# Kernel optimization log

Measured on AMD Instinct MI355X. Metric: run time of the kernel, lower is better.

## Reference

```python
import jax, jax.numpy as jnp
import numpy as np

H, NH, NKV, HD, I = 4096, 32, 8, 128, 14336
B, S = 1, 2048
THETA = 500000.0
EPS = 1e-5
SCALE = HD ** -0.5


def setup_inputs() -> dict:
    key = jax.random.key(0)
    ks = jax.random.split(key, 8)
    sc = 0.02
    return {
        "positions": jnp.arange(S, dtype=jnp.int32),
        "hidden_states": jax.random.normal(ks[0], (B, S, H), jnp.float32),
        "residual": jax.random.normal(ks[1], (B, S, H), jnp.float32),
        "w_qkv": jax.random.normal(ks[2], ((NH + 2 * NKV) * HD, H), jnp.float32) * sc,
        "w_o": jax.random.normal(ks[3], (H, NH * HD), jnp.float32) * sc,
        "w_gate_up": jax.random.normal(ks[4], (2 * I, H), jnp.float32) * sc,
        "w_down": jax.random.normal(ks[5], (H, I), jnp.float32) * sc,
        "w_ln1": jnp.ones((H,), jnp.float32),
        "w_ln2": jnp.ones((H,), jnp.float32),
    }


def rmsnorm(x, w):
    xf = x.astype(jnp.float32)
    y = xf * jax.lax.rsqrt(jnp.mean(xf * xf, axis=-1, keepdims=True) + EPS)
    return (y * w).astype(x.dtype)


def apply_rope(x, positions):
    # x: [B, S, nh, HD]; neox style: rotate halves
    half = HD // 2
    inv_freq = 1.0 / (THETA ** (jnp.arange(0, half, dtype=jnp.float32) / half))
    freqs = positions.astype(jnp.float32)[:, None] * inv_freq[None, :]  # [S, half]
    cos = jnp.cos(freqs)[None, :, None, :]
    sin = jnp.sin(freqs)[None, :, None, :]
    x1, x2 = x[..., :half], x[..., half:]
    return jnp.concatenate([x1 * cos - x2 * sin, x2 * cos + x1 * sin], axis=-1)


def reference(positions, hidden_states, residual, w_qkv, w_o, w_gate_up, w_down, w_ln1, w_ln2):
    # fused add + RMSNorm (input_layernorm with residual)
    residual = hidden_states + residual
    h = rmsnorm(residual, w_ln1)

    # fused QKV projection
    qkv = jnp.einsum('bsh,oh->bso', h, w_qkv)
    q = qkv[..., : NH * HD].reshape(B, S, NH, HD)
    k = qkv[..., NH * HD: (NH + NKV) * HD].reshape(B, S, NKV, HD)
    v = qkv[..., (NH + NKV) * HD:].reshape(B, S, NKV, HD)

    q = apply_rope(q, positions)
    k = apply_rope(k, positions)

    # GQA: expand kv heads
    rep = NH // NKV
    k = jnp.repeat(k, rep, axis=2)  # [B,S,NH,HD]
    v = jnp.repeat(v, rep, axis=2)

    scores = jnp.einsum('bqhd,bkhd->bhqk', q, k) * SCALE
    causal = jnp.tril(jnp.ones((S, S), bool))
    scores = jnp.where(causal[None, None], scores, jnp.float32(-1e30))
    attn = jax.nn.softmax(scores, axis=-1)
    ctx = jnp.einsum('bhqk,bkhd->bqhd', attn, v).reshape(B, S, NH * HD)
    attn_out = jnp.einsum('bso,ho->bsh', ctx, w_o)

    # fused add + RMSNorm (post_attention_layernorm)
    residual = attn_out + residual
    h = rmsnorm(residual, w_ln2)

    # SwiGLU MLP
    gu = jnp.einsum('bsh,oh->bso', h, w_gate_up)
    gate, up = gu[..., :I], gu[..., I:]
    h = jax.nn.silu(gate) * up
    out = jnp.einsum('bsi,hi->bsh', h, w_down)
    return out, residual
```

## Files before the change

kernel.cpp:

```cpp
#include <hip/hip_runtime.h>

typedef short bf16x8 __attribute__((ext_vector_type(8)));
typedef short short4v __attribute__((ext_vector_type(4)));
typedef float f32x4 __attribute__((ext_vector_type(4)));

#define SCALE_ATTN 0.08838834764831845f

__device__ inline short f2bs(float f) {
    unsigned u = __builtin_bit_cast(unsigned, f);
    unsigned r = (u + 0x7fffu + ((u >> 16) & 1u)) >> 16;
    return (short)(unsigned short)r;
}
__device__ inline float b2f(short s) {
    unsigned u = ((unsigned)(unsigned short)s) << 16;
    return __builtin_bit_cast(float, u);
}
__device__ inline void pack_w4(const f32x4& a, const f32x4& b, bf16x8& p) {
    p[0] = f2bs(a[0]); p[1] = f2bs(a[1]); p[2] = f2bs(a[2]); p[3] = f2bs(a[3]);
    p[4] = f2bs(b[0]); p[5] = f2bs(b[1]); p[6] = f2bs(b[2]); p[7] = f2bs(b[3]);
}

__global__ __launch_bounds__(256)
void wconv_kernel(const float* __restrict__ src, short* __restrict__ dst, long n8)
{
    const long stride = (long)gridDim.x << 8;
    for (long i = ((long)blockIdx.x << 8) + threadIdx.x; i < n8; i += stride) {
        const f32x4 a = __builtin_nontemporal_load(&((const f32x4*)src)[i << 1]);
        const f32x4 b = __builtin_nontemporal_load(&((const f32x4*)src)[(i << 1) + 1]);
        bf16x8 p;
        pack_w4(a, b, p);
        ((bf16x8*)dst)[i] = p;
    }
}

__global__ __launch_bounds__(512)
void wconv_gu_kernel(const float* __restrict__ src, short* __restrict__ dst)
{
    const int n = blockIdx.x;
    const int t = n >> 8, r = n & 255;
    const int orig = (r < 128) ? (t * 128 + r) : (14336 + t * 128 + (r - 128));
    const float* s = src + (long)orig * 4096;
    short* d = dst + (long)n * 4096;
    const int j = threadIdx.x << 3;
    f32x4 a = __builtin_nontemporal_load((const f32x4*)(s + j));
    f32x4 b = __builtin_nontemporal_load((const f32x4*)(s + j + 4));
    bf16x8 p; pack_w4(a, b, p);
    *(bf16x8*)(d + j) = p;
}

__global__ __launch_bounds__(256)
void add_rmsnorm_kernel(const float* __restrict__ X, const float* __restrict__ X2,
                        const float* __restrict__ Rin, const float* __restrict__ w,
                        float* __restrict__ Rout, short* __restrict__ Hout)
{
    const int tid = threadIdx.x;
    const long base = (long)blockIdx.x << 12;
    float v[16];
    float ss = 0.f;
#pragma unroll
    for (int p = 0; p < 4; ++p) {
        const int idx = (p << 10) + (tid << 2);
        f32x4 a = *(const f32x4*)(X + base + idx);
        if (X2 != nullptr) {
            f32x4 b = *(const f32x4*)(X2 + base + idx);
            a += b;
        }
        if (Rin != nullptr) {
            f32x4 b = *(const f32x4*)(Rin + base + idx);
            a += b;
        }
        v[p*4+0] = a[0]; v[p*4+1] = a[1]; v[p*4+2] = a[2]; v[p*4+3] = a[3];
        ss += a[0]*a[0] + a[1]*a[1] + a[2]*a[2] + a[3]*a[3];
    }
#pragma unroll
    for (int dd = 1; dd < 64; dd <<= 1) ss += __shfl_xor(ss, dd);
    __shared__ float red[4];
    if ((tid & 63) == 0) red[tid >> 6] = ss;
    __syncthreads();
    const float tot = red[0] + red[1] + red[2] + red[3];
    const float rstd = rsqrtf(tot * (1.0f / 4096.0f) + 1e-5f);
#pragma unroll
    for (int p = 0; p < 4; ++p) {
        const int idx = (p << 10) + (tid << 2);
        if (Rout != nullptr) {
            f32x4 b;
            b[0] = v[p*4+0]; b[1] = v[p*4+1]; b[2] = v[p*4+2]; b[3] = v[p*4+3];
            *(f32x4*)(Rout + base + idx) = b;
        }
        f32x4 wv4 = *(const f32x4*)(w + idx);
        short4v hb;
        hb[0] = f2bs(v[p*4+0] * rstd * wv4[0]);
        hb[1] = f2bs(v[p*4+1] * rstd * wv4[1]);
        hb[2] = f2bs(v[p*4+2] * rstd * wv4[2]);
        hb[3] = f2bs(v[p*4+3] * rstd * wv4[3]);
        *(short4v*)(Hout + base + idx) = hb;
    }
}

__global__ __launch_bounds__(256)
void add2_kernel(const float* __restrict__ a, const float* __restrict__ b,
                 float* __restrict__ o, long n4)
{
    const long st = (long)gridDim.x << 8;
    for (long i = ((long)blockIdx.x << 8) + threadIdx.x; i < n4; i += st) {
        f32x4 x = __builtin_nontemporal_load(&((const f32x4*)a)[i]);
        f32x4 y = __builtin_nontemporal_load(&((const f32x4*)b)[i]);
        x += y;
        ((f32x4*)o)[i] = x;
    }
}

#define BAR()   do { asm volatile("" ::: "memory"); __builtin_amdgcn_s_barrier(); asm volatile("" ::: "memory"); } while (0)
#define LGKM0() asm volatile("s_waitcnt lgkmcnt(0)" ::: "memory")
#define VMW(n)  asm volatile("s_waitcnt vmcnt(" #n ")" ::: "memory")

__device__ inline bf16x8 lds_frag(const short* tile, int row, int kb) {
    const int off = row * 128 + (kb ^ ((row & 7) << 4));
    return *(const bf16x8*)((const char*)tile + off);
}

__device__ inline void stage_half(const short* __restrict__ G, long grow0, long K,
                                  long k0, short* ldsHalf, int wv, int lane)
{
#pragma unroll
    for (int i = 0; i < 2; ++i) {
        short* dst = ldsHalf + ((i << 13) + (wv << 10)) / 2;
        const int off = (wv << 10) + (i << 13) + (lane << 4);
        const int r   = off >> 7;
        const int cb  = off & 127;
        const int gcb = cb ^ ((r & 7) << 4);
        const short* src = G + (grow0 + r) * K + k0 + (gcb >> 1);
        __builtin_amdgcn_global_load_lds(
            (const __attribute__((address_space(1))) void*)(const void*)src,
            (__attribute__((address_space(3))) void*)(void*)dst, 16, 0, 0);
    }
}

#define LOAD_A(T, grp) do {                                        \
    _Pragma("unroll") for (int _m = 0; _m < 4; ++_m) {             \
        const int _row = abase + (grp)*64 + _m*16 + l15;           \
        a[_m][0] = lds_frag(T, _row, l4b);                         \
        a[_m][1] = lds_frag(T, _row, 64 + l4b);                    \
    } } while (0)

#define LOAD_B(T, n0) do {                                         \
    _Pragma("unroll") for (int _n = 0; _n < 2; ++_n) {             \
        const int _row = bbase + ((n0)+_n)*16 + l15;               \
        b[(n0)+_n][0] = lds_frag(T, _row, l4b);                    \
        b[(n0)+_n][1] = lds_frag(T, _row, 64 + l4b);               \
    } } while (0)

#define MFMA16(MB, NB) do {                                                        \
    __builtin_amdgcn_s_setprio(1);                                                 \
    _Pragma("unroll") for (int _m = 0; _m < 4; ++_m)                               \
    _Pragma("unroll") for (int _n = 0; _n < 2; ++_n) {                             \
        acc[(MB)+_m][(NB)+_n] = __builtin_amdgcn_mfma_f32_16x16x32_bf16(           \
            a[_m][0], b[(NB)+_n][0], acc[(MB)+_m][(NB)+_n], 0, 0, 0);              \
        acc[(MB)+_m][(NB)+_n] = __builtin_amdgcn_mfma_f32_16x16x32_bf16(           \
            a[_m][1], b[(NB)+_n][1], acc[(MB)+_m][(NB)+_n], 0, 0, 0);              \
    }                                                                              \
    __builtin_amdgcn_s_setprio(0);                                                 \
} while (0)

template<int EPI, int KS>
__global__ __launch_bounds__(512, 2)
void gemm8(const short* __restrict__ A, const short* __restrict__ W,
           float* __restrict__ Cf, short* __restrict__ Cb,
           int N, int K)
{
    __shared__ __align__(16) short As[2][16384];
    __shared__ __align__(16) short Bs[2][16384];

    const int tid  = threadIdx.x;
    const int lane = tid & 63;
    const int wv   = tid >> 6;
    const int wm   = wv >> 2;
    const int wn   = wv & 3;
    const int l15  = lane & 15;
    const int l4b  = (lane >> 4) << 4;

    const int gx   = gridDim.x;
    const int nwg  = gx * 8 * KS;
    const int cpx  = nwg >> 3;
    const int orig = (blockIdx.z * 8 + blockIdx.y) * gx + blockIdx.x;
    const int lgc  = (orig & 7) * cpx + (orig >> 3);
    const int by   = lgc & 7;
    const int tq   = lgc >> 3;
    const int kz   = (KS == 1) ? 0 : (tq % KS);
    const int bx   = (KS == 1) ? tq : (tq / KS);

    const long row0 = (long)by << 8;
    const long col0 = (long)bx << 8;
    const int abase = wm << 7;
    const int bbase = wn << 6;

    const int  Kc    = K / KS;
    const long kbase = (long)kz * Kc;
    const int  iters = Kc >> 7;

    f32x4 acc[8][4];
#pragma unroll
    for (int i = 0; i < 8; ++i)
#pragma unroll
        for (int j = 0; j < 4; ++j) acc[i][j] = (f32x4){0.f,0.f,0.f,0.f};

    bf16x8 a[4][2], b[4][2];

    stage_half(A, row0,       K, kbase,      &As[0][0],    wv, lane);
    stage_half(A, row0 + 128, K, kbase,      &As[0][8192], wv, lane);
    stage_half(W, col0,       K, kbase,      &Bs[0][0],    wv, lane);
    stage_half(W, col0 + 128, K, kbase,      &Bs[0][8192], wv, lane);
    stage_half(A, row0,       K, kbase + 64, &As[1][0],    wv, lane);
    stage_half(A, row0 + 128, K, kbase + 64, &As[1][8192], wv, lane);
    stage_half(W, col0,       K, kbase + 64, &Bs[1][0],    wv, lane);
    stage_half(W, col0 + 128, K, kbase + 64, &Bs[1][8192], wv, lane);
    VMW(8);
    BAR();

#pragma unroll 1
    for (int it = 0; it < iters; ++it) {
        const long k2 = kbase + ((long)(2*it + 2) << 6);
        const long k3 = k2 + 64;
        const bool pf = (it + 1 < iters);

        LOAD_A(As[0], 0); LOAD_B(Bs[0], 0);
        BAR(); LGKM0(); MFMA16(0, 0); BAR();
        LOAD_B(Bs[0], 2);
        BAR(); LGKM0(); MFMA16(0, 2); BAR();
        LOAD_A(As[0], 1);
        if (pf) stage_half(W, col0, K, k2, &Bs[0][0], wv, lane);
        BAR(); LGKM0(); MFMA16(4, 0); BAR();
        if (pf) {
            stage_half(A, row0,       K, k2, &As[0][0],    wv, lane);
            stage_half(W, col0 + 128, K, k2, &Bs[0][8192], wv, lane);
        }
        VMW(6);
        BAR(); MFMA16(4, 2); BAR();

        LOAD_A(As[1], 0); LOAD_B(Bs[1], 0);
        if (pf) stage_half(A, row0 + 128, K, k2, &As[0][8192], wv, lane);
        BAR(); LGKM0(); MFMA16(0, 0); BAR();
        LOAD_B(Bs[1], 2);
        BAR(); LGKM0(); MFMA16(0, 2); BAR();
        LOAD_A(As[1], 1);
        if (pf) {
            stage_half(W, col0,       K, k3, &Bs[1][0],    wv, lane);
            stage_half(W, col0 + 128, K, k3, &Bs[1][8192], wv, lane);
        }
        BAR(); LGKM0(); MFMA16(4, 0); BAR();
        if (pf) {
            stage_half(A, row0,       K, k3, &As[1][0],    wv, lane);
            stage_half(A, row0 + 128, K, k3, &As[1][8192], wv, lane);
        }
        VMW(8);
        BAR(); MFMA16(4, 2); BAR();
    }

    if (EPI == 0) {
        float* Cfp = Cf + ((KS > 1) ? (long)kz * ((long)N << 11) : 0);
#pragma unroll
        for (int m = 0; m < 8; ++m) {
#pragma unroll
            for (int n = 0; n < 4; ++n) {
                const long gr = row0 + (wm << 7) + m*16 + ((lane >> 4) << 2);
                const long gc = col0 + (wn << 6) + n*16 + l15;
#pragma unroll
                for (int r = 0; r < 4; ++r)
                    Cfp[(gr + r) * N + gc] = acc[m][n][r];
            }
        }
    } else {
        float* eps = (float*)&As[0][0];
        const int r4 = (lane >> 4) << 2;
        const int rr = tid >> 4;
        const int cc = (tid & 15) << 3;
#pragma unroll 1
        for (int m = 0; m < 8; ++m) {
            __syncthreads();
#pragma unroll
            for (int n = 0; n < 4; ++n)
#pragma unroll
                for (int r = 0; r < 4; ++r)
                    eps[(wm*16 + r4 + r)*280 + (wn << 6) + n*16 + l15] = acc[m][n][r];
            __syncthreads();
            const float* rowp = eps + rr * 280;
            bf16x8 ov;
#pragma unroll
            for (int e = 0; e < 8; ++e) {
                const float g = rowp[cc + e];
                const float u = rowp[cc + 128 + e];
                ov[e] = f2bs(g / (1.f + __expf(-g)) * u);
            }
            const long grow = row0 + ((rr >> 4) << 7) + m*16 + (rr & 15);
            *(bf16x8*)(Cb + grow * N + (col0 >> 1) + cc) = ov;
        }
    }
}

__global__ __launch_bounds__(128)
void rope_kernel(const int* __restrict__ pos, const float* __restrict__ qkv,
                 short* __restrict__ Qo, short* __restrict__ Ko)
{
    const int h = blockIdx.x;
    const int s = blockIdx.y;
    const int d = threadIdx.x;
    const int j = d & 63;
    const float p = (float)pos[s];
    const float invf = __expf((float)j * -0.20503692895f);
    float sn, cs;
    __sincosf(p * invf, &sn, &cs);
    const long base = (long)s * 6144 + h * 128;
    const float x1 = qkv[base + j];
    const float x2 = qkv[base + 64 + j];
    const float outv = (d < 64) ? (x1 * cs - x2 * sn) : (x2 * cs + x1 * sn);
    const short ob = f2bs(outv);
    if (h < 32) Qo[(long)s * 4096 + h * 128 + d] = ob;
    else        Ko[(long)s * 1024 + (h - 32) * 128 + d] = ob;
}

__global__ __launch_bounds__(256)
void vtrans_kernel(const float* __restrict__ qkv, short* __restrict__ Vt)
{
    __shared__ short tile[64][136];
    const int tid = threadIdx.x;
    const int s0 = blockIdx.x << 6;
    const int h = blockIdx.y;
    {
        const int srow = tid >> 2;
        const int c0 = (tid & 3) << 5;
        const float* src = qkv + (long)(s0 + srow) * 6144 + 5120 + h * 128 + c0;
#pragma unroll
        for (int m = 0; m < 8; ++m) {
            f32x4 f = *(const f32x4*)(src + (m << 2));
            tile[srow][c0 + (m << 2) + 0] = f2bs(f[0]);
            tile[srow][c0 + (m << 2) + 1] = f2bs(f[1]);
            tile[srow][c0 + (m << 2) + 2] = f2bs(f[2]);
            tile[srow][c0 + (m << 2) + 3] = f2bs(f[3]);
        }
    }
    __syncthreads();
    {
        const int d = tid >> 1;
        const int sc = (tid & 1) << 5;
        short* dst = Vt + ((long)h * 128 + d) * 2048 + s0 + sc;
#pragma unroll
        for (int m = 0; m < 4; ++m) {
            bf16x8 v;
#pragma unroll
            for (int e = 0; e < 8; ++e) v[e] = tile[sc + (m << 3) + e][d];
            *(bf16x8*)(dst + (m << 3)) = v;
        }
    }
}

__global__ __launch_bounds__(256)
void flash_kernel(const short* __restrict__ Qg, const short* __restrict__ Kg,
                  const short* __restrict__ Vtg, short* __restrict__ Ctx)
{
    __shared__ short Qs[64 * 128];
    __shared__ short Ks[64 * 128];
    __shared__ short Vs[128 * 64];
    __shared__ short Ps[4 * 16 * 64];

    const int tid  = threadIdx.x;
    const int lane = tid & 63;
    const int wv   = tid >> 6;
    const int l15  = lane & 15;
    const int l4e  = (lane >> 4) << 3;
    const int qt   = blockIdx.x;
    const int head = blockIdx.y;
    const int q0   = qt << 6;
    const int kvh  = head >> 2;

    {
        const int row = tid >> 2;
        const int c0 = (tid & 3) << 5;
        const short* src = Qg + (long)(q0 + row) * 4096 + head * 128 + c0;
        const int sw = (row & 7) << 3;
#pragma unroll
        for (int m = 0; m < 4; ++m) {
            bf16x8 v = *(const bf16x8*)(src + (m << 3));
            *(bf16x8*)&Qs[row * 128 + ((c0 + (m << 3)) ^ sw)] = v;
        }
    }

    float mrow[4], lrow[4];
    f32x4 o[8];
#pragma unroll
    for (int r = 0; r < 4; ++r) { mrow[r] = -__builtin_inff(); lrow[r] = 0.f; }
#pragma unroll
    for (int d = 0; d < 8; ++d) o[d] = (f32x4){0.f,0.f,0.f,0.f};

    for (int t = 0; t <= qt; ++t) {
        const int kv0 = t << 6;
        __syncthreads();
        {
            const int row = tid >> 2;
            const int c0 = (tid & 3) << 5;
            const short* src = Kg + (long)(kv0 + row) * 1024 + kvh * 128 + c0;
            const int sw = (row & 7) << 3;
#pragma unroll
            for (int m = 0; m < 4; ++m) {
                bf16x8 v = *(const bf16x8*)(src + (m << 3));
                *(bf16x8*)&Ks[row * 128 + ((c0 + (m << 3)) ^ sw)] = v;
            }
        }
        {
            const int d = tid >> 1;
            const int c0 = (tid & 1) << 5;
            const short* src = Vtg + ((long)kvh * 128 + d) * 2048 + kv0 + c0;
            const int sw = (d & 7) << 3;
#pragma unroll
            for (int m = 0; m < 4; ++m) {
                bf16x8 v = *(const bf16x8*)(src + (m << 3));
                *(bf16x8*)&Vs[d * 64 + ((c0 + (m << 3)) ^ sw)] = v;
            }
        }
        __syncthreads();

        bf16x8 qa[4];
        {
            const int qrow = (wv << 4) + l15;
            const int sw = (qrow & 7) << 3;
#pragma unroll
            for (int kk = 0; kk < 4; ++kk)
                qa[kk] = *(const bf16x8*)&Qs[qrow * 128 + ((l4e + (kk << 5)) ^ sw)];
        }
        f32x4 sacc[4];
#pragma unroll
        for (int j = 0; j < 4; ++j) {
            sacc[j] = (f32x4){0.f,0.f,0.f,0.f};
            const int krow = (j << 4) + l15;
            const int sw = (krow & 7) << 3;
#pragma unroll
            for (int kk = 0; kk < 4; ++kk) {
                bf16x8 kb8 = *(const bf16x8*)&Ks[krow * 128 + ((l4e + (kk << 5)) ^ sw)];
                sacc[j] = __builtin_amdgcn_mfma_f32_16x16x32_bf16(qa[kk], kb8, sacc[j], 0, 0, 0);
            }
        }

#pragma unroll
        for (int ri = 0; ri < 4; ++ri) {
            const int grow = q0 + (wv << 4) + ((lane >> 4) << 2) + ri;
            float sv[4];
#pragma unroll
            for (int j = 0; j < 4; ++j) {
                float s = sacc[j][ri] * SCALE_ATTN;
                const int col = kv0 + (j << 4) + l15;
                sv[j] = (col > grow) ? -1e30f : s;
            }
            float mx = fmaxf(fmaxf(sv[0], sv[1]), fmaxf(sv[2], sv[3]));
#pragma unroll
            for (int dd = 1; dd < 16; dd <<= 1) mx = fmaxf(mx, __shfl_xor(mx, dd));
            const float mnew = fmaxf(mrow[ri], mx);
            const float alpha = __expf(mrow[ri] - mnew);
            mrow[ri] = mnew;
            float psum = 0.f;
            short pb[4];
#pragma unroll
            for (int j = 0; j < 4; ++j) {
                float p = __expf(sv[j] - mnew);
                psum += p;
                pb[j] = f2bs(p);
            }
            lrow[ri] = lrow[ri] * alpha + psum;
#pragma unroll
            for (int d = 0; d < 8; ++d) o[d][ri] *= alpha;
            const int prow = ((lane >> 4) << 2) + ri;
            const int sw = (prow & 7) << 3;
#pragma unroll
            for (int j = 0; j < 4; ++j)
                Ps[(wv << 10) + prow * 64 + ((((j << 4) + l15)) ^ sw)] = pb[j];
        }

        bf16x8 pa0, pa1;
        {
            const int prow = l15;
            const int sw = (prow & 7) << 3;
            pa0 = *(const bf16x8*)&Ps[(wv << 10) + prow * 64 + (l4e ^ sw)];
            pa1 = *(const bf16x8*)&Ps[(wv << 10) + prow * 64 + ((l4e + 32) ^ sw)];
        }
#pragma unroll
        for (int fd = 0; fd < 8; ++fd) {
            const int drow = (fd << 4) + l15;
            const int sw = (drow & 7) << 3;
            bf16x8 v0 = *(const bf16x8*)&Vs[drow * 64 + (l4e ^ sw)];
            bf16x8 v1 = *(const bf16x8*)&Vs[drow * 64 + ((l4e + 32) ^ sw)];
            o[fd] = __builtin_amdgcn_mfma_f32_16x16x32_bf16(pa0, v0, o[fd], 0, 0, 0);
            o[fd] = __builtin_amdgcn_mfma_f32_16x16x32_bf16(pa1, v1, o[fd], 0, 0, 0);
        }
    }

    float inv[4];
#pragma unroll
    for (int ri = 0; ri < 4; ++ri) {
        float ls = lrow[ri];
#pragma unroll
        for (int dd = 1; dd < 16; dd <<= 1) ls += __shfl_xor(ls, dd);
        inv[ri] = 1.0f / ls;
    }
#pragma unroll
    for (int fd = 0; fd < 8; ++fd)
#pragma unroll
        for (int ri = 0; ri < 4; ++ri) {
            const long row = q0 + (wv << 4) + ((lane >> 4) << 2) + ri;
            Ctx[row * 4096 + head * 128 + (fd << 4) + l15] = f2bs(o[fd][ri] * inv[ri]);
        }
}

extern "C" void kernel_launch(void* const* d_in, const int* in_sizes, int n_in,
                              void* d_out, int out_size, void* d_ws, size_t ws_size,
                              hipStream_t stream)
{
    const int*   positions = (const int*)d_in[0];
    const float* hidden    = (const float*)d_in[1];
    const float* residual  = (const float*)d_in[2];
    const float* w_qkv     = (const float*)d_in[3];
    const float* w_o       = (const float*)d_in[4];
    const float* w_gu      = (const float*)d_in[5];
    const float* w_down    = (const float*)d_in[6];
    const float* w_ln1     = (const float*)d_in[7];
    const float* w_ln2     = (const float*)d_in[8];

    float* out_f   = (float*)d_out;
    float* resid2  = out_f + 8388608;
    float* resid1  = out_f;

    char* wsb = (char*)d_ws;
    short* h1     = (short*)(wsb + 0);
    short* ctx    = (short*)(wsb + 0);
    float* qkvbuf = (float*)(wsb + 16777216);
    short* h2     = (short*)(wsb + 16777216);
    short* qb     = (short*)(wsb + 67108864);
    short* kb     = (short*)(wsb + 83886080);
    short* vt     = (short*)(wsb + 88080384);
    short* hm     = (short*)(wsb + 33554432);
    float* Po     = (float*)(wsb + 100663296);
    float* Pd     = (float*)(wsb + 100663296);
    short* wbuf   = (short*)(wsb + 209715200);
    short* wbuf_o = wbuf + 25165824;

    add_rmsnorm_kernel<<<2048, 256, 0, stream>>>(hidden, nullptr, residual, w_ln1, resid1, h1);
    wconv_kernel<<<2048, 256, 0, stream>>>(w_qkv, wbuf, 3145728L);
    gemm8<0,1><<<dim3(24, 8, 1), 512, 0, stream>>>(h1, wbuf, qkvbuf, nullptr, 6144, 4096);
    wconv_kernel<<<2048, 256, 0, stream>>>(w_o, wbuf_o, 2097152L);
    rope_kernel<<<dim3(40, 2048), 128, 0, stream>>>(positions, qkvbuf, qb, kb);
    vtrans_kernel<<<dim3(32, 8), 256, 0, stream>>>(qkvbuf, vt);
    flash_kernel<<<dim3(32, 32), 256, 0, stream>>>(qb, kb, vt, ctx);
    gemm8<0,2><<<dim3(16, 8, 2), 512, 0, stream>>>(ctx, wbuf_o, Po, nullptr, 4096, 4096);
    add_rmsnorm_kernel<<<2048, 256, 0, stream>>>(Po, Po + 8388608, resid1, w_ln2, resid2, h2);
    wconv_gu_kernel<<<28672, 512, 0, stream>>>(w_gu, wbuf);
    gemm8<3,1><<<dim3(112, 8, 1), 512, 0, stream>>>(h2, wbuf, nullptr, hm, 14336, 4096);
    wconv_kernel<<<2048, 256, 0, stream>>>(w_down, wbuf, 7340032L);
    gemm8<0,2><<<dim3(16, 8, 2), 512, 0, stream>>>(hm, wbuf, Pd, nullptr, 4096, 14336);
    add2_kernel<<<2048, 256, 0, stream>>>(Pd, Pd + 8388608, out_f, 2097152L);
}
```

Measured before the change: 1.447 ms.

## Unfuse SiLU epilogue from gate-up GEMM into separate elementwise kernel

Drops the interleaved gate/up weight conversion and the LDS-staged SiLU epilogue in the gate-up GEMM. The GEMM now writes the full bf16 gate|up output straight from registers, and a new silu_kernel combines gate and up into the MLP hidden buffer. Weight conversion stores become nontemporal, and workspace buffers are reassigned to fit the larger intermediate. The aim is to remove the epilogue's syncthreads and LDS round-trips and the row-gather conversion, at the cost of writing and rereading a 2048x28672 bf16 intermediate.

```diff
diff --git a/kernel.cpp b/kernel.cpp
--- a/kernel.cpp
+++ b/kernel.cpp
@@ -29,23 +29,8 @@
         const f32x4 b = __builtin_nontemporal_load(&((const f32x4*)src)[(i << 1) + 1]);
         bf16x8 p;
         pack_w4(a, b, p);
-        ((bf16x8*)dst)[i] = p;
-    }
-}
-
-__global__ __launch_bounds__(512)
-void wconv_gu_kernel(const float* __restrict__ src, short* __restrict__ dst)
-{
-    const int n = blockIdx.x;
-    const int t = n >> 8, r = n & 255;
-    const int orig = (r < 128) ? (t * 128 + r) : (14336 + t * 128 + (r - 128));
-    const float* s = src + (long)orig * 4096;
-    short* d = dst + (long)n * 4096;
-    const int j = threadIdx.x << 3;
-    f32x4 a = __builtin_nontemporal_load((const f32x4*)(s + j));
-    f32x4 b = __builtin_nontemporal_load((const f32x4*)(s + j + 4));
-    bf16x8 p; pack_w4(a, b, p);
-    *(bf16x8*)(d + j) = p;
+        __builtin_nontemporal_store(p, &((bf16x8*)dst)[i]);
+    }
 }
 
 __global__ __launch_bounds__(256)
@@ -108,6 +93,25 @@
         x += y;
         ((f32x4*)o)[i] = x;
     }
+}
+
+__global__ __launch_bounds__(256)
+void silu_kernel(const short* __restrict__ gu, short* __restrict__ hm)
+{
+    const int s = blockIdx.y;
+    const int j = ((blockIdx.x << 8) + threadIdx.x) << 3;
+    const short* g = gu + (long)s * 28672 + j;
+    bf16x8 gv = *(const bf16x8*)g;
+    bf16x8 uv = *(const bf16x8*)(g + 14336);
+    bf16x8 ov;
+#pragma unroll
+    for (int e = 0; e < 8; ++e) {
+        const float gf = b2f(gv[e]);
+        const float uf = b2f(uv[e]);
+        const float r = gf / (1.f + __expf(-gf)) * uf;
+        ov[e] = f2bs(r);
+    }
+    *(bf16x8*)(hm + (long)s * 14336 + j) = ov;
 }
 
 #define BAR()   do { asm volatile("" ::: "memory"); __builtin_amdgcn_s_barrier(); asm volatile("" ::: "memory"); } while (0)
@@ -270,29 +274,16 @@
             }
         }
     } else {
-        float* eps = (float*)&As[0][0];
-        const int r4 = (lane >> 4) << 2;
-        const int rr = tid >> 4;
-        const int cc = (tid & 15) << 3;
-#pragma unroll 1
+#pragma unroll
         for (int m = 0; m < 8; ++m) {
-            __syncthreads();
-#pragma unroll
-            for (int n = 0; n < 4; ++n)
+#pragma unroll
+            for (int n = 0; n < 4; ++n) {
+                const long gr = row0 + (wm << 7) + m*16 + ((lane >> 4) << 2);
+                const long gc = col0 + (wn << 6) + n*16 + l15;
 #pragma unroll
                 for (int r = 0; r < 4; ++r)
-                    eps[(wm*16 + r4 + r)*280 + (wn << 6) + n*16 + l15] = acc[m][n][r];
-            __syncthreads();
-            const float* rowp = eps + rr * 280;
-            bf16x8 ov;
-#pragma unroll
-            for (int e = 0; e < 8; ++e) {
-                const float g = rowp[cc + e];
-                const float u = rowp[cc + 128 + e];
-                ov[e] = f2bs(g / (1.f + __expf(-g)) * u);
-            }
-            const long grow = row0 + ((rr >> 4) << 7) + m*16 + (rr & 15);
-            *(bf16x8*)(Cb + grow * N + (col0 >> 1) + cc) = ov;
+                    Cb[(gr + r) * N + gc] = f2bs(acc[m][n][r]);
+            }
         }
     }
 }
@@ -534,9 +525,10 @@
     short* qb     = (short*)(wsb + 67108864);
     short* kb     = (short*)(wsb + 83886080);
     short* vt     = (short*)(wsb + 88080384);
-    short* hm     = (short*)(wsb + 33554432);
+    short* gu     = (short*)(wsb + 33554432);
+    short* hm     = (short*)(wsb + 150994944);
     float* Po     = (float*)(wsb + 100663296);
-    float* Pd     = (float*)(wsb + 100663296);
+    float* Pd     = (float*)(wsb + 0);
     short* wbuf   = (short*)(wsb + 209715200);
     short* wbuf_o = wbuf + 25165824;
 
@@ -549,8 +541,9 @@
     flash_kernel<<<dim3(32, 32), 256, 0, stream>>>(qb, kb, vt, ctx);
     gemm8<0,2><<<dim3(16, 8, 2), 512, 0, stream>>>(ctx, wbuf_o, Po, nullptr, 4096, 4096);
     add_rmsnorm_kernel<<<2048, 256, 0, stream>>>(Po, Po + 8388608, resid1, w_ln2, resid2, h2);
-    wconv_gu_kernel<<<28672, 512, 0, stream>>>(w_gu, wbuf);
-    gemm8<3,1><<<dim3(112, 8, 1), 512, 0, stream>>>(h2, wbuf, nullptr, hm, 14336, 4096);
+    wconv_kernel<<<2048, 256, 0, stream>>>(w_gu, wbuf, 14680064L);
+    gemm8<2,1><<<dim3(112, 8, 1), 512, 0, stream>>>(h2, wbuf, nullptr, gu, 28672, 4096);
+    silu_kernel<<<dim3(7, 2048), 256, 0, stream>>>(gu, hm);
     wconv_kernel<<<2048, 256, 0, stream>>>(w_down, wbuf, 7340032L);
     gemm8<0,2><<<dim3(16, 8, 2), 512, 0, stream>>>(hm, wbuf, Pd, nullptr, 4096, 14336);
     add2_kernel<<<2048, 256, 0, stream>>>(Pd, Pd + 8388608, out_f, 2097152L);
```

Result: faster. 1.383 ms (-4.4%).
